# Optimization experiments

Measured on AMD Instinct MI355X. Metric: run time of the kernel, lower is better.

The kernel has to match this reference:

```python
import jax, jax.numpy as jnp
import numpy as np

B, DIM, N = 4, 256, 2048
HEADS, DIM_HEAD = 8, 64
HIDDEN = HEADS * DIM_HEAD
SCALE = DIM_HEAD ** -0.5


def setup_inputs() -> dict:
    key = jax.random.key(0)
    k0, k1, k2, k3 = jax.random.split(key, 4)
    x = jax.random.normal(k0, (B, DIM, N), dtype=jnp.float32)
    # Conv1d kernel-size-1 weights == plain matrices over channels
    w_qkv = jax.random.normal(k1, (3 * HIDDEN, DIM), dtype=jnp.float32) * (DIM ** -0.5)
    w_out = jax.random.normal(k2, (DIM, HIDDEN), dtype=jnp.float32) * (HIDDEN ** -0.5)
    b_out = jax.random.normal(k3, (DIM,), dtype=jnp.float32) * 0.01
    return {"x": x, "w_qkv": w_qkv, "w_out": w_out, "b_out": b_out}


def reference(x, w_qkv, w_out, b_out):
    b, c, n = x.shape
    # 1x1 conv projection: [3H, C] x [b, C, n] -> [b, 3H, n]
    qkv = jnp.einsum('oc,bcn->bon', w_qkv, x)
    q, k, v = jnp.split(qkv, 3, axis=1)
    # [b, heads, dim_head, n]
    q = q.reshape(b, HEADS, DIM_HEAD, n) * SCALE
    k = k.reshape(b, HEADS, DIM_HEAD, n)
    v = v.reshape(b, HEADS, DIM_HEAD, n)
    sim = jnp.einsum('bhcn,bhcm->bhnm', q, k)          # [b,h,n,n]
    attn = jax.nn.softmax(sim, axis=-1)
    out = jnp.einsum('bhnm,bhcm->bhcn', attn, v)       # [b,h,dh,n]
    out = out.reshape(b, HIDDEN, n)
    return jnp.einsum('oc,bcn->bon', w_out, out) + b_out[None, :, None]
```

## Files before the change

kernel.cpp:

```cpp
#include <hip/hip_runtime.h>
#include <math.h>

#define BB 4
#define CDIM 256
#define NN 2048
#define HEADS 8
#define DH 64
#define HIDDEN 512
#define THREEH 1536
#define QSCALE 0.18033688011112042f

typedef __attribute__((ext_vector_type(8))) short bf16x8;
typedef __attribute__((ext_vector_type(4))) float f32x4;

static __device__ inline unsigned short f2bf(float f) {
    unsigned u = __float_as_uint(f);
    u += 0x7fff + ((u >> 16) & 1);
    return (unsigned short)(u >> 16);
}
#if __has_builtin(__builtin_amdgcn_cvt_pk_bf16_f32)
static __device__ inline unsigned pk2(float a, float b) {
    auto v = __builtin_amdgcn_cvt_pk_bf16_f32(a, b);
    return __builtin_bit_cast(unsigned, v);
}
#else
static __device__ inline unsigned pk2(float a, float b) {
    return (unsigned)f2bf(a) | ((unsigned)f2bf(b) << 16);
}
#endif
#if __has_builtin(__builtin_amdgcn_exp2f)
#define EXP2(x) __builtin_amdgcn_exp2f(x)
#else
#define EXP2(x) exp2f(x)
#endif
#define MFMA16(a, b, c) __builtin_amdgcn_mfma_f32_16x16x32_bf16(a, b, c, 0, 0, 0)
#define SWZC(row, ch) ((((ch) ^ ((row) & 7)) << 3))

__global__ __launch_bounds__(256) void prep_w(const float* __restrict__ wqkv,
                                              const float* __restrict__ wout,
                                              unsigned* __restrict__ Wqb,
                                              unsigned* __restrict__ Wob) {
    const int t = blockIdx.x * 256 + threadIdx.x;
    if (t < 98304) {
        const int e = t * 4;
        const int o = e >> 8;
        const float s = (o < HIDDEN) ? QSCALE : 1.f;
        float4 v = *(const float4*)&wqkv[e];
        Wqb[t * 2 + 0] = pk2(v.x * s, v.y * s);
        Wqb[t * 2 + 1] = pk2(v.z * s, v.w * s);
    } else {
        const int e = (t - 98304) * 4;
        float4 v = *(const float4*)&wout[e];
        Wob[(t - 98304) * 2 + 0] = pk2(v.x, v.y);
        Wob[(t - 98304) * 2 + 1] = pk2(v.z, v.w);
    }
}

__global__ __launch_bounds__(256) void prep_x(const float* __restrict__ x,
                                              unsigned short* __restrict__ Xt) {
    __shared__ float Ls[64][65];
    const int n0 = blockIdx.x * 64, c0 = blockIdx.y * 64, b = blockIdx.z;
    const int t = threadIdx.x;
    const int r16 = t >> 4, c16 = t & 15;
#pragma unroll
    for (int s = 0; s < 4; ++s) {
        const int c = s * 16 + r16;
        float4 v = *(const float4*)&x[((size_t)(b * CDIM + c0 + c)) * NN + n0 + c16 * 4];
        *(float4*)&Ls[c][c16 * 4] = v;
    }
    __syncthreads();
#pragma unroll
    for (int s = 0; s < 4; ++s) {
        const int n = s * 16 + r16;
        const int c4 = c16 * 4;
        uint2 u;
        u.x = pk2(Ls[c4][n], Ls[c4 + 1][n]);
        u.y = pk2(Ls[c4 + 2][n], Ls[c4 + 3][n]);
        *(uint2*)&Xt[((size_t)(b * NN) + n0 + n) * CDIM + c0 + c4] = u;
    }
}

__global__ __launch_bounds__(256, 3) void qkv_gemm(const unsigned short* __restrict__ Xt,
                                                   const unsigned short* __restrict__ Wqb,
                                                   unsigned short* __restrict__ Qb,
                                                   unsigned short* __restrict__ Kb,
                                                   unsigned short* __restrict__ Vb) {
    __shared__ unsigned short Xs[128 * 64], Ws[128 * 64];
    const int bn0 = blockIdx.x * 128, o0 = blockIdx.y * 128;
    const int t = threadIdx.x, l = t & 63, w = t >> 6, lo = l & 15, quad = l >> 4;
    const int wo = (w >> 1) * 64, wn = (w & 1) * 64;
    const int sr = t >> 1, scb = (t & 1) * 4;
    const bool isV = (o0 >= 2 * HIDDEN);
    f32x4 acc[4][4];
#pragma unroll
    for (int i = 0; i < 4; ++i)
#pragma unroll
        for (int j = 0; j < 4; ++j) acc[i][j] = (f32x4){0.f, 0.f, 0.f, 0.f};

    for (int kc = 0; kc < CDIM; kc += 64) {
        __syncthreads();
#pragma unroll
        for (int j = 0; j < 4; ++j) {
            const int ch = scb + j;
            *(uint4*)&Xs[sr * 64 + SWZC(sr, ch)] =
                *(const uint4*)&Xt[(size_t)(bn0 + sr) * CDIM + kc + ch * 8];
            *(uint4*)&Ws[sr * 64 + SWZC(sr, ch)] =
                *(const uint4*)&Wqb[(size_t)(o0 + sr) * CDIM + kc + ch * 8];
        }
        __syncthreads();
#pragma unroll
        for (int kk = 0; kk < 2; ++kk) {
            const int swz = SWZC(lo, kk * 4 + quad);
            if (!isV) {
                bf16x8 af[4], bv[4];
#pragma unroll
                for (int ot = 0; ot < 4; ++ot) af[ot] = *(const bf16x8*)&Ws[(wo + ot * 16 + lo) * 64 + swz];
#pragma unroll
                for (int nt = 0; nt < 4; ++nt) bv[nt] = *(const bf16x8*)&Xs[(wn + nt * 16 + lo) * 64 + swz];
#pragma unroll
                for (int ot = 0; ot < 4; ++ot)
#pragma unroll
                    for (int nt = 0; nt < 4; ++nt) acc[ot][nt] = MFMA16(af[ot], bv[nt], acc[ot][nt]);
            } else {
                bf16x8 af[4], bv[4];
#pragma unroll
                for (int mt = 0; mt < 4; ++mt) af[mt] = *(const bf16x8*)&Xs[(wn + mt * 16 + lo) * 64 + swz];
#pragma unroll
                for (int ot = 0; ot < 4; ++ot) bv[ot] = *(const bf16x8*)&Ws[(wo + ot * 16 + lo) * 64 + swz];
#pragma unroll
                for (int mt = 0; mt < 4; ++mt)
#pragma unroll
                    for (int ot = 0; ot < 4; ++ot) acc[mt][ot] = MFMA16(af[mt], bv[ot], acc[mt][ot]);
            }
        }
    }
    if (!isV) {
#pragma unroll
        for (int ot = 0; ot < 4; ++ot) {
            const int og = o0 + wo + ot * 16 + quad * 4;
            const int h = (og >> 6) & 7;
            const int c0 = og & 63;
            unsigned short* dst = (og >= HIDDEN) ? Kb : Qb;
#pragma unroll
            for (int nt = 0; nt < 4; ++nt) {
                const int bn = bn0 + wn + nt * 16 + lo;
                const int b = bn >> 11, n = bn & 2047;
                uint2 u;
                u.x = pk2(acc[ot][nt][0], acc[ot][nt][1]);
                u.y = pk2(acc[ot][nt][2], acc[ot][nt][3]);
                *(uint2*)&dst[(((size_t)(b * HEADS + h)) * NN + n) * DH + c0] = u;
            }
        }
    } else {
#pragma unroll
        for (int mt = 0; mt < 4; ++mt) {
            const int bn = bn0 + wn + mt * 16 + quad * 4;
            const int b = bn >> 11, m = bn & 2047;
#pragma unroll
            for (int ot = 0; ot < 4; ++ot) {
                const int og = o0 + wo + ot * 16 + lo;
                const int h = (og >> 6) & 7;
                const int c = og & 63;
                uint2 u;
                u.x = pk2(acc[mt][ot][0], acc[mt][ot][1]);
                u.y = pk2(acc[mt][ot][2], acc[mt][ot][3]);
                *(uint2*)&Vb[(((size_t)(b * HEADS + h)) * DH + c) * NN + m] = u;
            }
        }
    }
}

__global__ __launch_bounds__(256, 6) void flash_attn(const unsigned short* __restrict__ Qb,
                                                     const unsigned short* __restrict__ Kb,
                                                     const unsigned short* __restrict__ Vb,
                                                     unsigned short* __restrict__ Yb) {
    __shared__ unsigned short Ks[64 * 64], Vs[64 * 64], Ps[64 * 64];
    const int flat = blockIdx.x;
    const int rest = flat >> 3;
    const int bh = ((rest & 3) << 3) | (flat & 7);
    const int q0 = (rest >> 2) * 64;
    const int b = bh >> 3, h = bh & 7;
    const int t = threadIdx.x, l = t & 63, w = t >> 6, lo = l & 15, quad = l >> 4;
    const unsigned short* Qp = Qb + (size_t)bh * NN * DH;
    const unsigned short* Kp = Kb + (size_t)bh * NN * DH;
    const unsigned short* Vp = Vb + (size_t)bh * DH * NN;
    const int q = q0 + 16 * w + lo;
    const bf16x8 bQ0 = *(const bf16x8*)&Qp[(size_t)q * DH + quad * 8];
    const bf16x8 bQ1 = *(const bf16x8*)&Qp[(size_t)q * DH + 32 + quad * 8];
    f32x4 O[4];
#pragma unroll
    for (int i = 0; i < 4; ++i) O[i] = (f32x4){0.f, 0.f, 0.f, 0.f};
    float m_i = -INFINITY, l_i = 0.f;
    const int sr = t >> 3, sc = t & 7;
    const int kst0 = sr * 64 + SWZC(sr, sc);
    const int key = lo & 7;

    for (int m0 = 0; m0 < NN; m0 += 64) {
        __syncthreads();
        *(uint4*)&Ks[kst0]           = *(const uint4*)&Kp[(size_t)(m0 + sr) * DH + sc * 8];
        *(uint4*)&Ks[kst0 + 32 * 64] = *(const uint4*)&Kp[(size_t)(m0 + sr + 32) * DH + sc * 8];
        *(uint4*)&Vs[kst0]           = *(const uint4*)&Vp[(size_t)sr * NN + m0 + sc * 8];
        *(uint4*)&Vs[kst0 + 32 * 64] = *(const uint4*)&Vp[(size_t)(sr + 32) * NN + m0 + sc * 8];
        __syncthreads();
        f32x4 S[4];
#pragma unroll
        for (int nt = 0; nt < 4; ++nt) {
            const int rb = (nt * 16 + lo) * 64;
            bf16x8 a0 = *(const bf16x8*)&Ks[rb + SWZC(lo, quad)];
            bf16x8 a1 = *(const bf16x8*)&Ks[rb + SWZC(lo, quad + 4)];
            f32x4 z = (f32x4){0.f, 0.f, 0.f, 0.f};
            z = MFMA16(a0, bQ0, z);
            z = MFMA16(a1, bQ1, z);
            S[nt] = z;
        }
        float mx;
        {
            f32x4 mm;
#pragma unroll
            for (int i = 0; i < 4; ++i)
                mm[i] = fmaxf(fmaxf(S[0][i], S[1][i]), fmaxf(S[2][i], S[3][i]));
            mx = fmaxf(fmaxf(mm[0], mm[1]), fmaxf(mm[2], mm[3]));
        }
        mx = fmaxf(mx, __shfl_xor(mx, 16));
        mx = fmaxf(mx, __shfl_xor(mx, 32));
        const float mn = fmaxf(m_i, mx);
        const float alpha = EXP2(m_i - mn);
        m_i = mn;
        float ls = 0.f;
        const int prow = (16 * w + lo) * 64;
#pragma unroll
        for (int nt = 0; nt < 4; ++nt) {
            f32x4 p;
#pragma unroll
            for (int i = 0; i < 4; ++i) p[i] = EXP2(S[nt][i] - mn);
            ls += (p[0] + p[1]) + (p[2] + p[3]);
            uint2 u;
            u.x = pk2(p[0], p[1]);
            u.y = pk2(p[2], p[3]);
            *(uint2*)&Ps[prow + (((nt * 2 + (quad >> 1)) ^ key) << 3) + (quad & 1) * 4] = u;
        }
        ls += __shfl_xor(ls, 16);
        ls += __shfl_xor(ls, 32);
        l_i = l_i * alpha + ls;
        asm volatile("s_waitcnt lgkmcnt(0)" ::: "memory");
#pragma unroll
        for (int ct = 0; ct < 4; ++ct) O[ct] *= alpha;
        const bf16x8 pb0 = *(const bf16x8*)&Ps[prow + SWZC(lo, quad)];
        const bf16x8 pb1 = *(const bf16x8*)&Ps[prow + SWZC(lo, quad + 4)];
#pragma unroll
        for (int ct = 0; ct < 4; ++ct) {
            const int rb = (ct * 16 + lo) * 64;
            bf16x8 a0 = *(const bf16x8*)&Vs[rb + SWZC(lo, quad)];
            bf16x8 a1 = *(const bf16x8*)&Vs[rb + SWZC(lo, quad + 4)];
            O[ct] = MFMA16(a0, pb0, O[ct]);
            O[ct] = MFMA16(a1, pb1, O[ct]);
        }
    }
    const float inv = 1.f / l_i;
    unsigned short* yrow = Yb + (((size_t)(b * NN) + q)) * HIDDEN + h * DH;
#pragma unroll
    for (int ct = 0; ct < 4; ++ct) {
        uint2 u;
        u.x = pk2(O[ct][0] * inv, O[ct][1] * inv);
        u.y = pk2(O[ct][2] * inv, O[ct][3] * inv);
        *(uint2*)&yrow[ct * 16 + quad * 4] = u;
    }
}

__global__ __launch_bounds__(256, 4) void out_gemm(const unsigned short* __restrict__ Yb,
                                                   const unsigned short* __restrict__ Wob,
                                                   const float* __restrict__ bias,
                                                   float* __restrict__ out) {
    __shared__ unsigned short Ys[128 * 64], Wos[64 * 64];
    const int bn0 = blockIdx.x * 128, o0 = blockIdx.y * 64;
    const int t = threadIdx.x, l = t & 63, w = t >> 6, lo = l & 15, quad = l >> 4;
    const int wn = w * 32;
    const int sr = t >> 1, scb = (t & 1) * 4;
    const int sr2 = t >> 2, scb2 = (t & 3) * 2;
    f32x4 acc[2][4];
#pragma unroll
    for (int i = 0; i < 2; ++i)
#pragma unroll
        for (int j = 0; j < 4; ++j) acc[i][j] = (f32x4){0.f, 0.f, 0.f, 0.f};

    for (int kc = 0; kc < HIDDEN; kc += 64) {
        __syncthreads();
#pragma unroll
        for (int j = 0; j < 4; ++j) {
            const int ch = scb + j;
            *(uint4*)&Ys[sr * 64 + SWZC(sr, ch)] =
                *(const uint4*)&Yb[(size_t)(bn0 + sr) * HIDDEN + kc + ch * 8];
        }
#pragma unroll
        for (int j = 0; j < 2; ++j) {
            const int ch = scb2 + j;
            *(uint4*)&Wos[sr2 * 64 + SWZC(sr2, ch)] =
                *(const uint4*)&Wob[(size_t)(o0 + sr2) * HIDDEN + kc + ch * 8];
        }
        __syncthreads();
#pragma unroll
        for (int kk = 0; kk < 2; ++kk) {
            const int swz = SWZC(lo, kk * 4 + quad);
            bf16x8 bv[4];
#pragma unroll
            for (int ot = 0; ot < 4; ++ot) bv[ot] = *(const bf16x8*)&Wos[(ot * 16 + lo) * 64 + swz];
#pragma unroll
            for (int mt = 0; mt < 2; ++mt) {
                bf16x8 av = *(const bf16x8*)&Ys[(wn + mt * 16 + lo) * 64 + swz];
#pragma unroll
                for (int ot = 0; ot < 4; ++ot) acc[mt][ot] = MFMA16(av, bv[ot], acc[mt][ot]);
            }
        }
    }
#pragma unroll
    for (int mt = 0; mt < 2; ++mt) {
        const int bn = bn0 + wn + mt * 16 + quad * 4;
        const int b = bn >> 11, n = bn & 2047;
#pragma unroll
        for (int ot = 0; ot < 4; ++ot) {
            const int o = o0 + ot * 16 + lo;
            *(f32x4*)&out[((size_t)(b * CDIM + o)) * NN + n] = acc[mt][ot] + bias[o];
        }
    }
}

extern "C" void kernel_launch(void* const* d_in, const int* in_sizes, int n_in,
                              void* d_out, int out_size, void* d_ws, size_t ws_size,
                              hipStream_t stream) {
    const float* x     = (const float*)d_in[0];
    const float* w_qkv = (const float*)d_in[1];
    const float* w_out = (const float*)d_in[2];
    const float* b_out = (const float*)d_in[3];
    float* out = (float*)d_out;

    unsigned short* Wqb = (unsigned short*)d_ws;
    unsigned short* Wob = Wqb + (size_t)THREEH * CDIM;
    unsigned short* Xt  = Wob + (size_t)CDIM * HIDDEN;
    unsigned short* Qb  = Xt + (size_t)BB * NN * CDIM;
    unsigned short* Kb  = Qb + (size_t)BB * HEADS * NN * DH;
    unsigned short* Vb  = Kb + (size_t)BB * HEADS * NN * DH;
    unsigned short* Yb  = Vb + (size_t)BB * HEADS * DH * NN;

    prep_w<<<512, 256, 0, stream>>>(w_qkv, w_out, (unsigned*)Wqb, (unsigned*)Wob);
    prep_x<<<dim3(NN / 64, CDIM / 64, BB), 256, 0, stream>>>(x, Xt);
    qkv_gemm<<<dim3(BB * NN / 128, THREEH / 128), 256, 0, stream>>>(Xt, Wqb, Qb, Kb, Vb);
    flash_attn<<<1024, 256, 0, stream>>>(Qb, Kb, Vb, Yb);
    out_gemm<<<dim3(BB * NN / 128, CDIM / 64), 256, 0, stream>>>(Yb, Wob, b_out, out);
}
```

Before: 164.7 us.

## Split KV across waves in flash attention and merge partial softmax results

The attention kernel is restructured so each wave owns all 64 query rows and a separate 64-key slice of each 256-key step. K and V fragments are loaded directly from global memory into registers instead of being staged through shared memory, which removes the per-tile block barriers. The per-wave partial outputs, maxima and sums are merged through a large shared buffer at the end. Rescaling of O is skipped when no row's max changed. The cost is much higher register and shared-memory use, with occupancy dropping from 6 to 2 blocks per CU, plus uncoalesced direct global loads.

Measured after the change: 168.8 us. +2.5%, slower.

```diff
diff --git a/kernel.cpp b/kernel.cpp
--- a/kernel.cpp
+++ b/kernel.cpp
@@ -170,101 +170,162 @@
     }
 }
 
-__global__ __launch_bounds__(256, 6) void flash_attn(const unsigned short* __restrict__ Qb,
+__global__ __launch_bounds__(256, 2) void flash_attn(const unsigned short* __restrict__ Qb,
                                                      const unsigned short* __restrict__ Kb,
                                                      const unsigned short* __restrict__ Vb,
                                                      unsigned short* __restrict__ Yb) {
-    __shared__ unsigned short Ks[64 * 64], Vs[64 * 64], Ps[64 * 64];
+    __shared__ char smem[71680];
     const int flat = blockIdx.x;
     const int rest = flat >> 3;
     const int bh = ((rest & 3) << 3) | (flat & 7);
     const int q0 = (rest >> 2) * 64;
     const int b = bh >> 3, h = bh & 7;
     const int t = threadIdx.x, l = t & 63, w = t >> 6, lo = l & 15, quad = l >> 4;
+    unsigned short* Pw = (unsigned short*)smem + (size_t)w * 4096;
+    float* OpF = (float*)smem;
+    float* mM = (float*)(smem + 69632);
+    float* mL = mM + 256;
     const unsigned short* Qp = Qb + (size_t)bh * NN * DH;
     const unsigned short* Kp = Kb + (size_t)bh * NN * DH;
     const unsigned short* Vp = Vb + (size_t)bh * DH * NN;
-    const int q = q0 + 16 * w + lo;
-    const bf16x8 bQ0 = *(const bf16x8*)&Qp[(size_t)q * DH + quad * 8];
-    const bf16x8 bQ1 = *(const bf16x8*)&Qp[(size_t)q * DH + 32 + quad * 8];
-    f32x4 O[4];
-#pragma unroll
-    for (int i = 0; i < 4; ++i) O[i] = (f32x4){0.f, 0.f, 0.f, 0.f};
-    float m_i = -INFINITY, l_i = 0.f;
-    const int sr = t >> 3, sc = t & 7;
-    const int kst0 = sr * 64 + SWZC(sr, sc);
     const int key = lo & 7;
 
-    for (int m0 = 0; m0 < NN; m0 += 64) {
-        __syncthreads();
-        *(uint4*)&Ks[kst0]           = *(const uint4*)&Kp[(size_t)(m0 + sr) * DH + sc * 8];
-        *(uint4*)&Ks[kst0 + 32 * 64] = *(const uint4*)&Kp[(size_t)(m0 + sr + 32) * DH + sc * 8];
-        *(uint4*)&Vs[kst0]           = *(const uint4*)&Vp[(size_t)sr * NN + m0 + sc * 8];
-        *(uint4*)&Vs[kst0 + 32 * 64] = *(const uint4*)&Vp[(size_t)(sr + 32) * NN + m0 + sc * 8];
-        __syncthreads();
-        f32x4 S[4];
+    bf16x8 bQ[4][2];
+#pragma unroll
+    for (int qt = 0; qt < 4; ++qt)
+#pragma unroll
+        for (int hh = 0; hh < 2; ++hh)
+            bQ[qt][hh] = *(const bf16x8*)&Qp[(size_t)(q0 + qt * 16 + lo) * DH + hh * 32 + quad * 8];
+
+    f32x4 O[4][4];
+#pragma unroll
+    for (int i = 0; i < 4; ++i)
+#pragma unroll
+        for (int j = 0; j < 4; ++j) O[i][j] = (f32x4){0.f, 0.f, 0.f, 0.f};
+    float m_i[4], l_i[4];
+#pragma unroll
+    for (int qt = 0; qt < 4; ++qt) { m_i[qt] = -INFINITY; l_i[qt] = 0.f; }
+
+#pragma unroll 1
+    for (int m0 = 0; m0 < NN; m0 += 256) {
+        const int mw = m0 + w * 64;
+        bf16x8 aK0[4], aK1[4];
 #pragma unroll
         for (int nt = 0; nt < 4; ++nt) {
-            const int rb = (nt * 16 + lo) * 64;
-            bf16x8 a0 = *(const bf16x8*)&Ks[rb + SWZC(lo, quad)];
-            bf16x8 a1 = *(const bf16x8*)&Ks[rb + SWZC(lo, quad + 4)];
-            f32x4 z = (f32x4){0.f, 0.f, 0.f, 0.f};
-            z = MFMA16(a0, bQ0, z);
-            z = MFMA16(a1, bQ1, z);
-            S[nt] = z;
-        }
-        float mx;
-        {
-            f32x4 mm;
-#pragma unroll
-            for (int i = 0; i < 4; ++i)
-                mm[i] = fmaxf(fmaxf(S[0][i], S[1][i]), fmaxf(S[2][i], S[3][i]));
-            mx = fmaxf(fmaxf(mm[0], mm[1]), fmaxf(mm[2], mm[3]));
-        }
-        mx = fmaxf(mx, __shfl_xor(mx, 16));
-        mx = fmaxf(mx, __shfl_xor(mx, 32));
-        const float mn = fmaxf(m_i, mx);
-        const float alpha = EXP2(m_i - mn);
-        m_i = mn;
-        float ls = 0.f;
-        const int prow = (16 * w + lo) * 64;
-#pragma unroll
-        for (int nt = 0; nt < 4; ++nt) {
-            f32x4 p;
-#pragma unroll
-            for (int i = 0; i < 4; ++i) p[i] = EXP2(S[nt][i] - mn);
-            ls += (p[0] + p[1]) + (p[2] + p[3]);
-            uint2 u;
-            u.x = pk2(p[0], p[1]);
-            u.y = pk2(p[2], p[3]);
-            *(uint2*)&Ps[prow + (((nt * 2 + (quad >> 1)) ^ key) << 3) + (quad & 1) * 4] = u;
-        }
-        ls += __shfl_xor(ls, 16);
-        ls += __shfl_xor(ls, 32);
-        l_i = l_i * alpha + ls;
+            const unsigned short* kr = Kp + (size_t)(mw + nt * 16 + lo) * DH + quad * 8;
+            aK0[nt] = *(const bf16x8*)kr;
+            aK1[nt] = *(const bf16x8*)(kr + 32);
+        }
+        f32x4 S[4][4];
+#pragma unroll
+        for (int nt = 0; nt < 4; ++nt)
+#pragma unroll
+            for (int qt = 0; qt < 4; ++qt) {
+                f32x4 z = (f32x4){0.f, 0.f, 0.f, 0.f};
+                z = MFMA16(aK0[nt], bQ[qt][0], z);
+                z = MFMA16(aK1[nt], bQ[qt][1], z);
+                S[nt][qt] = z;
+            }
+        float alpha[4];
+#pragma unroll
+        for (int qt = 0; qt < 4; ++qt) {
+            float mx;
+            {
+                f32x4 mm;
+#pragma unroll
+                for (int i = 0; i < 4; ++i)
+                    mm[i] = fmaxf(fmaxf(S[0][qt][i], S[1][qt][i]), fmaxf(S[2][qt][i], S[3][qt][i]));
+                mx = fmaxf(fmaxf(mm[0], mm[1]), fmaxf(mm[2], mm[3]));
+            }
+            mx = fmaxf(mx, __shfl_xor(mx, 16));
+            mx = fmaxf(mx, __shfl_xor(mx, 32));
+            const float mn = fmaxf(m_i[qt], mx);
+            alpha[qt] = EXP2(m_i[qt] - mn);
+            m_i[qt] = mn;
+            float ls = 0.f;
+            const int prow = (qt * 16 + lo) * 64;
+#pragma unroll
+            for (int nt = 0; nt < 4; ++nt) {
+                f32x4 p;
+#pragma unroll
+                for (int i = 0; i < 4; ++i) p[i] = EXP2(S[nt][qt][i] - mn);
+                ls += (p[0] + p[1]) + (p[2] + p[3]);
+                uint2 u;
+                u.x = pk2(p[0], p[1]);
+                u.y = pk2(p[2], p[3]);
+                *(uint2*)&Pw[prow + (((nt * 2 + (quad >> 1)) ^ key) << 3) + (quad & 1) * 4] = u;
+            }
+            ls += __shfl_xor(ls, 16);
+            ls += __shfl_xor(ls, 32);
+            l_i[qt] = l_i[qt] * alpha[qt] + ls;
+        }
         asm volatile("s_waitcnt lgkmcnt(0)" ::: "memory");
-#pragma unroll
-        for (int ct = 0; ct < 4; ++ct) O[ct] *= alpha;
-        const bf16x8 pb0 = *(const bf16x8*)&Ps[prow + SWZC(lo, quad)];
-        const bf16x8 pb1 = *(const bf16x8*)&Ps[prow + SWZC(lo, quad + 4)];
-#pragma unroll
-        for (int ct = 0; ct < 4; ++ct) {
-            const int rb = (ct * 16 + lo) * 64;
-            bf16x8 a0 = *(const bf16x8*)&Vs[rb + SWZC(lo, quad)];
-            bf16x8 a1 = *(const bf16x8*)&Vs[rb + SWZC(lo, quad + 4)];
-            O[ct] = MFMA16(a0, pb0, O[ct]);
-            O[ct] = MFMA16(a1, pb1, O[ct]);
-        }
-    }
-    const float inv = 1.f / l_i;
-    unsigned short* yrow = Yb + (((size_t)(b * NN) + q)) * HIDDEN + h * DH;
-#pragma unroll
-    for (int ct = 0; ct < 4; ++ct) {
-        uint2 u;
-        u.x = pk2(O[ct][0] * inv, O[ct][1] * inv);
-        u.y = pk2(O[ct][2] * inv, O[ct][3] * inv);
-        *(uint2*)&yrow[ct * 16 + quad * 4] = u;
-    }
+        const float am = fminf(fminf(alpha[0], alpha[1]), fminf(alpha[2], alpha[3]));
+        if (__ballot(am < 1.f)) {
+#pragma unroll
+            for (int ct = 0; ct < 4; ++ct)
+#pragma unroll
+                for (int qt = 0; qt < 4; ++qt) O[ct][qt] *= alpha[qt];
+        }
+#pragma unroll
+        for (int kk = 0; kk < 2; ++kk) {
+            bf16x8 pb[4];
+#pragma unroll
+            for (int qt = 0; qt < 4; ++qt)
+                pb[qt] = *(const bf16x8*)&Pw[(qt * 16 + lo) * 64 + (((kk * 4 + quad) ^ key) << 3)];
+            bf16x8 aV[4];
+#pragma unroll
+            for (int ct = 0; ct < 4; ++ct)
+                aV[ct] = *(const bf16x8*)&Vp[(size_t)(ct * 16 + lo) * NN + mw + kk * 32 + quad * 8];
+#pragma unroll
+            for (int ct = 0; ct < 4; ++ct)
+#pragma unroll
+                for (int qt = 0; qt < 4; ++qt) O[ct][qt] = MFMA16(aV[ct], pb[qt], O[ct][qt]);
+        }
+    }
+
+    if (quad == 0) {
+#pragma unroll
+        for (int qt = 0; qt < 4; ++qt) {
+            mM[w * 64 + qt * 16 + lo] = m_i[qt];
+            mL[w * 64 + qt * 16 + lo] = l_i[qt];
+        }
+    }
+    __syncthreads();
+    float fsc[4];
+#pragma unroll
+    for (int qt = 0; qt < 4; ++qt) {
+        const int qi = qt * 16 + lo;
+        float ms = fmaxf(fmaxf(mM[qi], mM[64 + qi]), fmaxf(mM[128 + qi], mM[192 + qi]));
+        fsc[qt] = EXP2(m_i[qt] - ms);
+    }
+#pragma unroll
+    for (int ct = 0; ct < 4; ++ct)
+#pragma unroll
+        for (int qt = 0; qt < 4; ++qt) {
+            f32x4 v = O[ct][qt] * fsc[qt];
+            *(f32x4*)&OpF[(size_t)(w * 64 + qt * 16 + lo) * 68 + ct * 16 + quad * 4] = v;
+        }
+    __syncthreads();
+    const int qi = l;
+    float ms = fmaxf(fmaxf(mM[qi], mM[64 + qi]), fmaxf(mM[128 + qi], mM[192 + qi]));
+    float lstar = EXP2(mM[qi] - ms) * mL[qi] + EXP2(mM[64 + qi] - ms) * mL[64 + qi] +
+                  EXP2(mM[128 + qi] - ms) * mL[128 + qi] + EXP2(mM[192 + qi] - ms) * mL[192 + qi];
+    const float inv = 1.f / lstar;
+    unsigned uo[8];
+#pragma unroll
+    for (int j = 0; j < 4; ++j) {
+        f32x4 s = (f32x4){0.f, 0.f, 0.f, 0.f};
+#pragma unroll
+        for (int wp = 0; wp < 4; ++wp)
+            s += *(const f32x4*)&OpF[(size_t)(wp * 64 + qi) * 68 + 16 * w + j * 4];
+        s *= inv;
+        uo[2 * j]     = pk2(s[0], s[1]);
+        uo[2 * j + 1] = pk2(s[2], s[3]);
+    }
+    unsigned short* yp = Yb + ((size_t)(b * NN) + q0 + qi) * HIDDEN + h * DH + 16 * w;
+    *(uint4*)&yp[0] = *(uint4*)&uo[0];
+    *(uint4*)&yp[8] = *(uint4*)&uo[4];
 }
 
 __global__ __launch_bounds__(256, 4) void out_gemm(const unsigned short* __restrict__ Yb,
```
